# Kernel optimization log

Measured on AMD Instinct MI355X. Metric: run time of the kernel, lower is better.

## Reference

```python
import jax, jax.numpy as jnp
import numpy as np

B, C, O, N, T, K = 4, 64, 64, 32768, 4, 9
PAD, DIL = 4, 1  # padding*dilation, dilation
SIGMA = 0.05
EPS_BN = 1e-5


def _gather_ch(x, idx):
    # x: [B, C, N], idx: [B, N] -> gather along last dim per channel
    idx3 = jnp.broadcast_to(idx[:, None, :], x.shape)
    return jnp.take_along_axis(x, idx3, axis=-1)


def _weighted_conv(x, coords, w):
    # x: [B,C,N], coords: [B,3,N], w: [O,C,K]
    xp = jnp.pad(x, ((0, 0), (0, 0), (PAD, PAD)))
    cp = jnp.pad(coords, ((0, 0), (0, 0), (PAD, PAD)))
    win_idx = jnp.arange(N)[:, None] + jnp.arange(K) * DIL  # [N, K]
    win = xp[:, :, win_idx]   # [B,C,N,K]
    cwin = cp[:, :, win_idx]  # [B,3,N,K]
    d = cwin - cwin[:, :, :, K // 2:K // 2 + 1]
    s = jnp.sum(d * d, axis=1)                    # [B,N,K]
    r = jnp.sqrt(jnp.where(s > 0, s, 1.0))
    r = jnp.where(s > 0, r, 0.0)
    wgt = jnp.maximum(1.0 - r / SIGMA, 0.0)       # [B,N,K]
    return jnp.einsum('bcnk,bnk,ock->bon', win, wgt, w)


def _bn(x, g, b):
    # training-mode BatchNorm1d over (B, N)
    m = jnp.mean(x, axis=(0, 2), keepdims=True)
    v = jnp.var(x, axis=(0, 2), keepdims=True)
    return g[None, :, None] * (x - m) * jax.lax.rsqrt(v + EPS_BN) + b[None, :, None]


def setup_inputs() -> dict:
    key = jax.random.key(0)
    ks = jax.random.split(key, 12)
    inp = jax.random.normal(ks[0], (B, C, N), dtype=jnp.float32)
    # coords in a small box so sigma=0.05 yields non-trivial weights
    multi_coords = jax.random.uniform(ks[1], (B, 3, N, T), dtype=jnp.float32) * 0.02
    indices = jax.random.randint(ks[2], (B, N, T), 0, N, dtype=jnp.int32)
    reindices = jax.random.randint(ks[3], (B, N, T), 0, N, dtype=jnp.int32)
    fan = C * K
    conv_w = jax.random.normal(ks[4], (T, O, C, K), dtype=jnp.float32) / np.sqrt(fan)
    bn_gamma = jnp.ones((T, O), dtype=jnp.float32)
    bn_beta = jnp.zeros((T, O), dtype=jnp.float32)
    fusion_w = jax.random.normal(ks[5], (O, T * O), dtype=jnp.float32) / np.sqrt(T * O)
    fusion_b = jnp.zeros((O,), dtype=jnp.float32)
    fusion_gamma = jnp.ones((O,), dtype=jnp.float32)
    fusion_beta = jnp.zeros((O,), dtype=jnp.float32)
    return {"input": inp, "multi_coords": multi_coords, "indices": indices,
            "reindices": reindices, "conv_w": conv_w, "bn_gamma": bn_gamma,
            "bn_beta": bn_beta, "fusion_w": fusion_w, "fusion_b": fusion_b,
            "fusion_gamma": fusion_gamma, "fusion_beta": fusion_beta}


def reference(input, multi_coords, indices, reindices, conv_w, bn_gamma, bn_beta,
              fusion_w, fusion_b, fusion_gamma, fusion_beta):
    outs = []
    for i in range(T):  # fixed small set of 4 Hilbert orders
        x = _gather_ch(input, indices[:, :, i])            # [B,C,N]
        x = _weighted_conv(x, multi_coords[:, :, :, i], conv_w[i])  # [B,O,N]
        x = _bn(x, bn_gamma[i], bn_beta[i])
        x = _gather_ch(x, reindices[:, :, i])
        outs.append(x)
    cat = jnp.concatenate(outs, axis=1)                    # [B, T*O, N]
    y = jnp.einsum('bcn,oc->bon', cat, fusion_w) + fusion_b[None, :, None]
    y = _bn(y, fusion_gamma, fusion_beta)
    return jax.nn.relu(y)
```

## Files before the change

### kernel.cpp

```cpp
#include <hip/hip_runtime.h>
#include <hip/hip_bf16.h>

#define BB 4
#define CC 64
#define OO 64
#define NN 32768
#define TT 4
#define KK 9
#define PADW 4
#define SIGMA 0.05f
#define EPS_BN 1e-5f

typedef __attribute__((ext_vector_type(8))) short bf16x8;
typedef __attribute__((ext_vector_type(4))) float f32x4;

__device__ __forceinline__ unsigned short f2bf(float f) {
  __hip_bfloat16 h = __float2bfloat16(f);
  return *reinterpret_cast<unsigned short*>(&h);
}
__device__ __forceinline__ float bf2f(unsigned short u) {
  unsigned int x = ((unsigned int)u) << 16;
  float f;
  __builtin_memcpy(&f, &x, 4);
  return f;
}
__device__ __forceinline__ unsigned int pkbf(float a, float b) {
  float2 t; t.x = a; t.y = b;
  __hip_bfloat162 h = __float22bfloat162_rn(t);
  unsigned int r;
  __builtin_memcpy(&r, &h, 4);
  return r;
}

__global__ __launch_bounds__(256) void transpose_kernel(
    const float* __restrict__ inp, unsigned short* __restrict__ xTb)
{
  const int n0 = blockIdx.x * 64;
  const int b  = blockIdx.y;
  const int tid = threadIdx.x;
  __shared__ float xt[64][65];
  {
    int nl = tid & 63, c4 = tid >> 6;
    #pragma unroll
    for (int i = 0; i < 16; ++i) {
      int c = c4 * 16 + i;
      xt[c][nl] = inp[((size_t)(b*CC + c))*NN + n0 + nl];
    }
  }
  __syncthreads();
  {
    int nl = tid >> 2, cq = tid & 3;
    unsigned int pk[8];
    #pragma unroll
    for (int i = 0; i < 8; ++i) {
      int c = cq*16 + i*2;
      pk[i] = pkbf(xt[c][nl], xt[c+1][nl]);
    }
    unsigned int* dst = (unsigned int*)(xTb + (((size_t)b*NN) + n0 + nl)*CC + cq*16);
    ((int4*)dst)[0] = make_int4((int)pk[0],(int)pk[1],(int)pk[2],(int)pk[3]);
    ((int4*)dst)[1] = make_int4((int)pk[4],(int)pk[5],(int)pk[6],(int)pk[7]);
  }
}

__global__ __launch_bounds__(256) void wprep_kernel(
    const float* __restrict__ cw, unsigned short* __restrict__ W4)
{
  const int k = blockIdx.x;
  const int t = blockIdx.y;
  for (int u = threadIdx.x; u < OO*CC; u += 256) {
    int o = u >> 6, c = u & 63;
    int ow = o >> 5, ot = (o >> 4) & 1, l15 = o & 15;
    int frag = c >> 5, q = (c >> 3) & 3, j = c & 7;
    float wv = cw[(((size_t)(t*OO + o))*CC + c)*KK + k];
    W4[(size_t)(t*9+k)*4096 + ow*2048 + ot*1024 + frag*512 + l15*32 + q*8 + j]
        = f2bf(wv);
  }
}

__global__ __launch_bounds__(256, 4) void conv_kernel(
    const unsigned short* __restrict__ xTb,
    const float* __restrict__ mc,
    const int*   __restrict__ ind,
    const unsigned short* __restrict__ W4,
    unsigned short* __restrict__ Y,
    float* __restrict__ cpart2)
{
  const int n0  = blockIdx.x * 128;
  const int b   = blockIdx.y;
  const int t   = blockIdx.z;
  const int tid = threadIdx.x;
  const int lane = tid & 63;
  const int w    = tid >> 6;
  const int l15  = lane & 15;
  const int q    = lane >> 4;
  const int ow   = w & 1;
  const int nw   = w >> 1;

  __shared__ short xg[136][72];
  __shared__ float wgl[128][10];
  __shared__ float mcs[3][140];

  int4 g[5];
  #pragma unroll
  for (int i = 0; i < 5; ++i) {
    int u = tid + 256*i;
    g[i] = make_int4(0,0,0,0);
    if (u < 1088) {
      int p = u >> 3, s = u & 7;
      int m = n0 + p - PADW;
      if (m >= 0 && m < NN) {
        int idx = ind[((size_t)b*NN + m)*TT + t];
        g[i] = *(const int4*)(xTb + ((size_t)b*NN + idx)*CC + s*8);
      }
    }
  }

  if (tid < 136) {
    int m = n0 + tid - PADW;
    #pragma unroll
    for (int d = 0; d < 3; ++d) {
      float4 v = make_float4(0.f, 0.f, 0.f, 0.f);
      if (m >= 0 && m < NN)
        v = *(const float4*)(mc + (((size_t)(b*3+d))*NN + m)*TT);
      mcs[d][tid] = (t==0) ? v.x : (t==1) ? v.y : (t==2) ? v.z : v.w;
    }
  }

  #pragma unroll
  for (int i = 0; i < 5; ++i) {
    int u = tid + 256*i;
    if (u < 1088) {
      int p = u >> 3, s = u & 7;
      *(int4*)&xg[p][s*8] = g[i];
    }
  }
  __syncthreads();

  {
    int nl = tid >> 1;
    int k0 = (tid & 1) * 5;
    int kc = 5 - (tid & 1);
    float cx = mcs[0][nl+4], cy = mcs[1][nl+4], cz = mcs[2][nl+4];
    for (int i2 = 0; i2 < kc; ++i2) {
      int k = k0 + i2, mi = nl + k;
      float dx = mcs[0][mi]-cx, dy = mcs[1][mi]-cy, dz = mcs[2][mi]-cz;
      float s2 = dx*dx + dy*dy + dz*dz;
      float r = (s2 > 0.f) ? sqrtf(s2) : 0.f;
      wgl[nl][k] = fmaxf(1.f - r*(1.f/SIGMA), 0.f);
    }
  }
  __syncthreads();

  const unsigned short* Wt = W4 + (size_t)t*9*4096 + ow*2048 + (l15*4 + q)*8;
  const f32x4 Z = {0.f, 0.f, 0.f, 0.f};
  f32x4 fin[2][4];
  #pragma unroll
  for (int ot = 0; ot < 2; ++ot)
    #pragma unroll
    for (int ns = 0; ns < 4; ++ns) fin[ot][ns] = Z;

  for (int k = 0; k < KK; ++k) {
    const unsigned short* Wk = Wt + (size_t)k*4096;
    bf16x8 af[2][2];
    #pragma unroll
    for (int ot = 0; ot < 2; ++ot) {
      af[ot][0] = *(const bf16x8*)(Wk + ot*1024);
      af[ot][1] = *(const bf16x8*)(Wk + ot*1024 + 512);
    }
    #pragma unroll
    for (int ns = 0; ns < 4; ++ns) {
      int nl = nw*64 + ns*16 + l15;
      int p  = nl + k;
      bf16x8 b0 = *(const bf16x8*)&xg[p][q*8];
      bf16x8 b1 = *(const bf16x8*)&xg[p][32 + q*8];
      float wgt = wgl[nl][k];
      #pragma unroll
      for (int ot = 0; ot < 2; ++ot) {
        f32x4 d = __builtin_amdgcn_mfma_f32_16x16x32_bf16(af[ot][0], b0, Z, 0, 0, 0);
        d = __builtin_amdgcn_mfma_f32_16x16x32_bf16(af[ot][1], b1, d, 0, 0, 0);
        fin[ot][ns] += wgt * d;
      }
    }
  }

  #pragma unroll
  for (int ns = 0; ns < 4; ++ns) {
    int nl = nw*64 + ns*16 + l15;
    size_t row = (((size_t)t*BB + b)*NN + n0 + nl)*OO;
    #pragma unroll
    for (int ot = 0; ot < 2; ++ot) {
      uint2 pk2;
      pk2.x = pkbf(fin[ot][ns][0], fin[ot][ns][1]);
      pk2.y = pkbf(fin[ot][ns][2], fin[ot][ns][3]);
      *(uint2*)(Y + row + ow*32 + ot*16 + q*4) = pk2;
    }
  }

  float sv[16];
  #pragma unroll
  for (int ot = 0; ot < 2; ++ot)
    #pragma unroll
    for (int r = 0; r < 4; ++r) {
      float a = 0.f, qs = 0.f;
      #pragma unroll
      for (int ns = 0; ns < 4; ++ns) {
        float v = fin[ot][ns][r];
        a += v; qs += v*v;
      }
      sv[ot*4+r] = a; sv[8+ot*4+r] = qs;
    }
  #pragma unroll
  for (int msk = 1; msk < 16; msk <<= 1) {
    #pragma unroll
    for (int i = 0; i < 16; ++i) sv[i] += __shfl_xor(sv[i], msk, 16);
  }
  if (l15 == 0) {
    int slot4 = ((b*256 + (int)blockIdx.x) << 2) | w;
    #pragma unroll
    for (int ot = 0; ot < 2; ++ot)
      #pragma unroll
      for (int r = 0; r < 4; ++r) {
        int o = ow*32 + ot*16 + q*4 + r;
        cpart2[((size_t)((t*64 + o)*2 + 0))*4096 + slot4] = sv[ot*4+r];
        cpart2[((size_t)((t*64 + o)*2 + 1))*4096 + slot4] = sv[8+ot*4+r];
      }
  }
}

__global__ __launch_bounds__(256) void bnparam_kernel(
    const float* __restrict__ cpart2,
    const float* __restrict__ gam,
    const float* __restrict__ bet,
    float* __restrict__ ss)
{
  const int to = blockIdx.x;
  const int tid = threadIdx.x;
  __shared__ float r1[256], r2[256];
  const float* p1 = cpart2 + (size_t)to*2*4096;
  const float* p2 = p1 + 4096;
  float s1 = 0.f, s2 = 0.f;
  for (int i = tid*4; i < 4096; i += 1024) {
    float4 a = *(const float4*)(p1 + i);
    float4 c = *(const float4*)(p2 + i);
    s1 += a.x + a.y + a.z + a.w;
    s2 += c.x + c.y + c.z + c.w;
  }
  r1[tid] = s1; r2[tid] = s2;
  __syncthreads();
  for (int st = 128; st > 0; st >>= 1) {
    if (tid < st) { r1[tid] += r1[tid+st]; r2[tid] += r2[tid+st]; }
    __syncthreads();
  }
  if (tid == 0) {
    const float inv = 1.f / (float)(BB * NN);
    float mean = r1[0] * inv;
    float var  = r2[0] * inv - mean * mean;
    float sc = gam[to] * rsqrtf(var + EPS_BN);
    ss[to*2 + 0] = sc;
    ss[to*2 + 1] = bet[to] - mean * sc;
  }
}

__global__ void bias2_kernel(
    const float* __restrict__ fw, const float* __restrict__ ss,
    const float* __restrict__ fb, float* __restrict__ bias2)
{
  int o = threadIdx.x;
  float s = fb[o];
  for (int c = 0; c < 256; ++c) s += fw[o*256 + c] * ss[c*2 + 1];
  bias2[o] = s;
}

__global__ __launch_bounds__(256) void fusion_kernel(
    const unsigned short* __restrict__ Y,
    const int*   __restrict__ rind,
    const float* __restrict__ ss,
    const float* __restrict__ fw,
    const float* __restrict__ bias2,
    float* __restrict__ out)
{
  const int n0  = blockIdx.x * 128;
  const int b   = blockIdx.y;
  const int tid = threadIdx.x;
  const int lane = tid & 63;
  const int w    = tid >> 6;
  const int l15  = lane & 15;
  const int q    = lane >> 4;
  const int ow   = w & 1;
  const int nw   = w >> 1;

  __shared__ int   rnl[TT][128];
  __shared__ float scl[256];
  __shared__ float b2l[64];

  if (tid < 128) {
    int4 r4 = *(const int4*)(rind + ((size_t)b*NN + n0 + tid)*TT);
    rnl[0][tid] = r4.x; rnl[1][tid] = r4.y;
    rnl[2][tid] = r4.z; rnl[3][tid] = r4.w;
  }
  scl[tid] = ss[tid*2];
  if (tid < 64) b2l[tid] = bias2[tid];
  __syncthreads();

  f32x4 fin[2][4];
  #pragma unroll
  for (int ot = 0; ot < 2; ++ot)
    #pragma unroll
    for (int ns = 0; ns < 4; ++ns) fin[ot][ns] = (f32x4){0.f,0.f,0.f,0.f};

  for (int r = 0; r < 4; ++r) {
    const unsigned short* Yb = Y + ((size_t)r*BB + b)*NN*OO;
    #pragma unroll
    for (int kk = 0; kk < 2; ++kk) {
      bf16x8 af[2];
      #pragma unroll
      for (int ot = 0; ot < 2; ++ot) {
        const float* wp = fw + (size_t)(ow*32 + ot*16 + l15)*256 + r*64 + kk*32 + q*8;
        const float* sp = scl + r*64 + kk*32 + q*8;
        unsigned int pk[4];
        #pragma unroll
        for (int j = 0; j < 4; ++j)
          pk[j] = pkbf(wp[2*j]*sp[2*j], wp[2*j+1]*sp[2*j+1]);
        int4 tmp = make_int4((int)pk[0],(int)pk[1],(int)pk[2],(int)pk[3]);
        __builtin_memcpy(&af[ot], &tmp, 16);
      }
      #pragma unroll
      for (int ns = 0; ns < 4; ++ns) {
        int nl = nw*64 + ns*16 + l15;
        int rn = rnl[r][nl];
        bf16x8 braw = *(const bf16x8*)(Yb + (size_t)rn*OO + kk*32 + q*8);
        #pragma unroll
        for (int ot = 0; ot < 2; ++ot)
          fin[ot][ns] = __builtin_amdgcn_mfma_f32_16x16x32_bf16(af[ot], braw, fin[ot][ns], 0, 0, 0);
      }
    }
  }

  #pragma unroll
  for (int ot = 0; ot < 2; ++ot)
    #pragma unroll
    for (int rr = 0; rr < 4; ++rr) {
      int o = ow*32 + ot*16 + q*4 + rr;
      float bias = b2l[o];
      float* dst = out + ((size_t)(b*OO + o))*NN + n0 + nw*64;
      #pragma unroll
      for (int ns = 0; ns < 4; ++ns)
        dst[ns*16 + l15] = fin[ot][ns][rr] + bias;
    }
}

__global__ __launch_bounds__(256) void fstat_kernel(
    const float* __restrict__ out, float* __restrict__ fpart)
{
  const int o = blockIdx.x, b = blockIdx.y;
  const int tid = threadIdx.x;
  __shared__ float r1[256], r2[256];
  const float* src = out + ((size_t)(b*OO + o))*NN;
  float s1 = 0.f, s2 = 0.f;
  for (int i = tid*4; i < NN; i += 1024) {
    float4 v = *(const float4*)(src + i);
    s1 += v.x + v.y + v.z + v.w;
    s2 += v.x*v.x + v.y*v.y + v.z*v.z + v.w*v.w;
  }
  r1[tid] = s1; r2[tid] = s2;
  __syncthreads();
  for (int st = 128; st > 0; st >>= 1) {
    if (tid < st) { r1[tid] += r1[tid+st]; r2[tid] += r2[tid+st]; }
    __syncthreads();
  }
  if (tid == 0) {
    fpart[(b*OO + o)*2 + 0] = r1[0];
    fpart[(b*OO + o)*2 + 1] = r2[0];
  }
}

__global__ void freduce_kernel(
    const float* __restrict__ fpart,
    const float* __restrict__ fg,
    const float* __restrict__ fbeta,
    float* __restrict__ fss)
{
  int o = threadIdx.x;
  float s1 = 0.f, s2 = 0.f;
  #pragma unroll
  for (int b = 0; b < BB; ++b) {
    s1 += fpart[(b*OO + o)*2 + 0];
    s2 += fpart[(b*OO + o)*2 + 1];
  }
  const float inv = 1.f / (float)(BB * NN);
  float mean = s1 * inv;
  float var  = s2 * inv - mean * mean;
  float sc = fg[o] * rsqrtf(var + EPS_BN);
  fss[o*2 + 0] = sc;
  fss[o*2 + 1] = fbeta[o] - mean * sc;
}

__global__ __launch_bounds__(256) void final_kernel(
    float* __restrict__ out, const float* __restrict__ fss)
{
  const size_t base = (size_t)blockIdx.x * 2048 + threadIdx.x * 4;
  #pragma unroll
  for (int s = 0; s < 2; ++s) {
    size_t e = base + (size_t)s * 1024;
    int o2 = (int)((e >> 15) & 63);
    float sc = fss[o2*2 + 0];
    float sh = fss[o2*2 + 1];
    float4 v = *(float4*)(out + e);
    v.x = fmaxf(v.x*sc + sh, 0.f);
    v.y = fmaxf(v.y*sc + sh, 0.f);
    v.z = fmaxf(v.z*sc + sh, 0.f);
    v.w = fmaxf(v.w*sc + sh, 0.f);
    *(float4*)(out + e) = v;
  }
}

extern "C" void kernel_launch(void* const* d_in, const int* in_sizes, int n_in,
                              void* d_out, int out_size, void* d_ws, size_t ws_size,
                              hipStream_t stream) {
  const float* inp  = (const float*)d_in[0];
  const float* mc   = (const float*)d_in[1];
  const int*   ind  = (const int*)  d_in[2];
  const int*   rind = (const int*)  d_in[3];
  const float* cw   = (const float*)d_in[4];
  const float* bg   = (const float*)d_in[5];
  const float* bb   = (const float*)d_in[6];
  const float* fw   = (const float*)d_in[7];
  const float* fb   = (const float*)d_in[8];
  const float* fg   = (const float*)d_in[9];
  const float* fbt  = (const float*)d_in[10];

  char* ws = (char*)d_ws;
  float* convss = (float*)(ws + 0);
  float* fss    = (float*)(ws + 2048);
  float* fpart  = (float*)(ws + 2560);
  float* bias2  = (float*)(ws + 4608);
  unsigned short* Y = (unsigned short*)(ws + 8192);

  char* ob = (char*)d_out;
  unsigned short* xTb = (unsigned short*)ob;
  unsigned short* W4  = (unsigned short*)(ob + 16777216);
  float*          cpart2 = (float*)(ob + 17072128);
  float* out = (float*)d_out;

  dim3 gt(NN/64, BB);
  transpose_kernel<<<gt, 256, 0, stream>>>(inp, xTb);

  dim3 gw(KK, TT);
  wprep_kernel<<<gw, 256, 0, stream>>>(cw, W4);

  dim3 gc(NN/128, BB, TT);
  conv_kernel<<<gc, 256, 0, stream>>>(xTb, mc, ind, W4, Y, cpart2);

  bnparam_kernel<<<256, 256, 0, stream>>>(cpart2, bg, bb, convss);

  bias2_kernel<<<1, 64, 0, stream>>>(fw, convss, fb, bias2);

  dim3 gf(NN/128, BB);
  fusion_kernel<<<gf, 256, 0, stream>>>(Y, rind, convss, fw, bias2, out);

  dim3 gs(OO, BB);
  fstat_kernel<<<gs, 256, 0, stream>>>(out, fpart);

  freduce_kernel<<<1, 64, 0, stream>>>(fpart, fg, fbt, fss);

  final_kernel<<<(BB*OO*NN)/2048, 256, 0, stream>>>(out, fss);
}
```

Baseline: 254.2 us.

## Fold tiny bias and BN-reduce kernels into consumers; stage gathered Y rows in LDS

Removes the single-block bias2 and freduce kernels by recomputing the folded bias inside each fusion block and the final BN scale/shift inside each final_kernel block, cutting two serial launches. The fusion kernel now stages the gathered Y rows for each order into shared memory with coalesced 16-byte loads before the MFMA loop, replacing scattered per-lane global reads. The cost is redundant per-block recomputation of the bias (a 256-wide dot product per output channel in every block) and extra barriers per order.

```diff
diff --git a/kernel.cpp b/kernel.cpp
--- a/kernel.cpp
+++ b/kernel.cpp
@@ -17,12 +17,6 @@
 __device__ __forceinline__ unsigned short f2bf(float f) {
   __hip_bfloat16 h = __float2bfloat16(f);
   return *reinterpret_cast<unsigned short*>(&h);
-}
-__device__ __forceinline__ float bf2f(unsigned short u) {
-  unsigned int x = ((unsigned int)u) << 16;
-  float f;
-  __builtin_memcpy(&f, &x, 4);
-  return f;
 }
 __device__ __forceinline__ unsigned int pkbf(float a, float b) {
   float2 t; t.x = a; t.y = b;
@@ -261,22 +255,12 @@
   }
 }
 
-__global__ void bias2_kernel(
-    const float* __restrict__ fw, const float* __restrict__ ss,
-    const float* __restrict__ fb, float* __restrict__ bias2)
-{
-  int o = threadIdx.x;
-  float s = fb[o];
-  for (int c = 0; c < 256; ++c) s += fw[o*256 + c] * ss[c*2 + 1];
-  bias2[o] = s;
-}
-
 __global__ __launch_bounds__(256) void fusion_kernel(
     const unsigned short* __restrict__ Y,
     const int*   __restrict__ rind,
     const float* __restrict__ ss,
     const float* __restrict__ fw,
-    const float* __restrict__ bias2,
+    const float* __restrict__ fb,
     float* __restrict__ out)
 {
   const int n0  = blockIdx.x * 128;
@@ -289,9 +273,11 @@
   const int ow   = w & 1;
   const int nw   = w >> 1;
 
+  __shared__ short zg[128][72];
   __shared__ int   rnl[TT][128];
   __shared__ float scl[256];
   __shared__ float b2l[64];
+  __shared__ float bred[4][64];
 
   if (tid < 128) {
     int4 r4 = *(const int4*)(rind + ((size_t)b*NN + n0 + tid)*TT);
@@ -299,8 +285,16 @@
     rnl[2][tid] = r4.z; rnl[3][tid] = r4.w;
   }
   scl[tid] = ss[tid*2];
-  if (tid < 64) b2l[tid] = bias2[tid];
-  __syncthreads();
+  {
+    int o = tid & 63, g = tid >> 6;
+    const float* wp = fw + (size_t)o*256 + g*64;
+    float s = 0.f;
+    for (int j = 0; j < 64; ++j) s += wp[j] * ss[(g*64 + j)*2 + 1];
+    bred[g][o] = s;
+  }
+  __syncthreads();
+  if (tid < 64)
+    b2l[tid] = fb[tid] + bred[0][tid] + bred[1][tid] + bred[2][tid] + bred[3][tid];
 
   f32x4 fin[2][4];
   #pragma unroll
@@ -309,7 +303,17 @@
     for (int ns = 0; ns < 4; ++ns) fin[ot][ns] = (f32x4){0.f,0.f,0.f,0.f};
 
   for (int r = 0; r < 4; ++r) {
+    if (r) __syncthreads();
     const unsigned short* Yb = Y + ((size_t)r*BB + b)*NN*OO;
+    #pragma unroll
+    for (int i = 0; i < 4; ++i) {
+      int u = tid + 256*i;
+      int n = u >> 3, s = u & 7;
+      int rn = rnl[r][n];
+      *(int4*)&zg[n][s*8] = *(const int4*)(Yb + (size_t)rn*OO + s*8);
+    }
+    __syncthreads();
+
     #pragma unroll
     for (int kk = 0; kk < 2; ++kk) {
       bf16x8 af[2];
@@ -327,11 +331,10 @@
       #pragma unroll
       for (int ns = 0; ns < 4; ++ns) {
         int nl = nw*64 + ns*16 + l15;
-        int rn = rnl[r][nl];
-        bf16x8 braw = *(const bf16x8*)(Yb + (size_t)rn*OO + kk*32 + q*8);
+        bf16x8 bfr = *(const bf16x8*)&zg[nl][kk*32 + q*8];
         #pragma unroll
         for (int ot = 0; ot < 2; ++ot)
-          fin[ot][ns] = __builtin_amdgcn_mfma_f32_16x16x32_bf16(af[ot], braw, fin[ot][ns], 0, 0, 0);
+          fin[ot][ns] = __builtin_amdgcn_mfma_f32_16x16x32_bf16(af[ot], bfr, fin[ot][ns], 0, 0, 0);
       }
     }
   }
@@ -374,37 +377,34 @@
   }
 }
 
-__global__ void freduce_kernel(
-    const float* __restrict__ fpart,
-    const float* __restrict__ fg,
-    const float* __restrict__ fbeta,
-    float* __restrict__ fss)
-{
-  int o = threadIdx.x;
-  float s1 = 0.f, s2 = 0.f;
-  #pragma unroll
-  for (int b = 0; b < BB; ++b) {
-    s1 += fpart[(b*OO + o)*2 + 0];
-    s2 += fpart[(b*OO + o)*2 + 1];
-  }
-  const float inv = 1.f / (float)(BB * NN);
-  float mean = s1 * inv;
-  float var  = s2 * inv - mean * mean;
-  float sc = fg[o] * rsqrtf(var + EPS_BN);
-  fss[o*2 + 0] = sc;
-  fss[o*2 + 1] = fbeta[o] - mean * sc;
-}
-
 __global__ __launch_bounds__(256) void final_kernel(
-    float* __restrict__ out, const float* __restrict__ fss)
-{
-  const size_t base = (size_t)blockIdx.x * 2048 + threadIdx.x * 4;
+    float* __restrict__ out, const float* __restrict__ fpart,
+    const float* __restrict__ fg, const float* __restrict__ fbeta)
+{
+  __shared__ float fssl[128];
+  const int tid = threadIdx.x;
+  if (tid < 64) {
+    float s1 = 0.f, s2 = 0.f;
+    #pragma unroll
+    for (int b = 0; b < BB; ++b) {
+      s1 += fpart[(b*OO + tid)*2 + 0];
+      s2 += fpart[(b*OO + tid)*2 + 1];
+    }
+    const float inv = 1.f / (float)(BB * NN);
+    float mean = s1 * inv;
+    float var  = s2 * inv - mean * mean;
+    float sc = fg[tid] * rsqrtf(var + EPS_BN);
+    fssl[tid*2 + 0] = sc;
+    fssl[tid*2 + 1] = fbeta[tid] - mean * sc;
+  }
+  __syncthreads();
+  const size_t base = (size_t)blockIdx.x * 2048 + tid * 4;
   #pragma unroll
   for (int s = 0; s < 2; ++s) {
     size_t e = base + (size_t)s * 1024;
     int o2 = (int)((e >> 15) & 63);
-    float sc = fss[o2*2 + 0];
-    float sh = fss[o2*2 + 1];
+    float sc = fssl[o2*2 + 0];
+    float sh = fssl[o2*2 + 1];
     float4 v = *(float4*)(out + e);
     v.x = fmaxf(v.x*sc + sh, 0.f);
     v.y = fmaxf(v.y*sc + sh, 0.f);
@@ -431,9 +431,7 @@
 
   char* ws = (char*)d_ws;
   float* convss = (float*)(ws + 0);
-  float* fss    = (float*)(ws + 2048);
   float* fpart  = (float*)(ws + 2560);
-  float* bias2  = (float*)(ws + 4608);
   unsigned short* Y = (unsigned short*)(ws + 8192);
 
   char* ob = (char*)d_out;
@@ -453,15 +451,11 @@
 
   bnparam_kernel<<<256, 256, 0, stream>>>(cpart2, bg, bb, convss);
 
-  bias2_kernel<<<1, 64, 0, stream>>>(fw, convss, fb, bias2);
-
   dim3 gf(NN/128, BB);
-  fusion_kernel<<<gf, 256, 0, stream>>>(Y, rind, convss, fw, bias2, out);
+  fusion_kernel<<<gf, 256, 0, stream>>>(Y, rind, convss, fw, fb, out);
 
   dim3 gs(OO, BB);
   fstat_kernel<<<gs, 256, 0, stream>>>(out, fpart);
 
-  freduce_kernel<<<1, 64, 0, stream>>>(fpart, fg, fbt, fss);
-
-  final_kernel<<<(BB*OO*NN)/2048, 256, 0, stream>>>(out, fss);
-}
+  final_kernel<<<(BB*OO*NN)/2048, 256, 0, stream>>>(out, fpart, fg, fbt);
+}
```

Measured after the change: 242.8 us. 1.05x faster.
